# Kernel tuning notes

Measured on AMD Instinct MI355X. Metric: run time of the kernel, lower is better.

The kernel has to match this reference:

```python
import jax, jax.numpy as jnp
import numpy as np

R = 4
D = 2 * R + 1  # 9
B, C, H, W = 1, 256, 48, 96


def setup_inputs() -> dict:
    key = jax.random.key(0)
    k1, k2, k3, k4, k5 = jax.random.split(key, 5)
    f1 = jax.random.normal(k1, (B, C, H, W), dtype=jnp.float32)
    f2 = jax.random.normal(k2, (B, C, H, W), dtype=jnp.float32)
    cx = jax.random.uniform(k3, (B, H, W), dtype=jnp.float32) * (W - 1)
    cy = jax.random.uniform(k4, (B, H, W), dtype=jnp.float32) * (H - 1)
    coords = jnp.stack([cx, cy], axis=1)  # (B,2,H,W), ch0=x, ch1=y
    # DAP: 1x1 conv over (2r+1)^2 channels, identity init (perturbed so it is non-trivial)
    w_dap = jnp.eye(D * D, dtype=jnp.float32) + 0.02 * jax.random.normal(k5, (D * D, D * D), dtype=jnp.float32)
    return {"f1": f1, "f2": f2, "coords": coords, "w_dap": w_dap}


def _bilinear_sample(img, px, py):
    # img: (C,H,W); px,py: (M,) pixel coords; zeros padding, align_corners=True semantics
    c, h, w = img.shape
    x0 = jnp.floor(px)
    y0 = jnp.floor(py)
    x1 = x0 + 1.0
    y1 = y0 + 1.0
    wx1 = px - x0
    wx0 = 1.0 - wx1
    wy1 = py - y0
    wy0 = 1.0 - wy1
    flat = img.reshape(c, h * w)

    def corner(xi, yi, wgt):
        valid = (xi >= 0) & (xi <= w - 1) & (yi >= 0) & (yi <= h - 1)
        xc = jnp.clip(xi, 0, w - 1).astype(jnp.int32)
        yc = jnp.clip(yi, 0, h - 1).astype(jnp.int32)
        v = flat[:, yc * w + xc]  # (C,M)
        return v * (wgt * valid.astype(wgt.dtype))[None, :]

    return (corner(x0, y0, wx0 * wy0) + corner(x1, y0, wx1 * wy0)
            + corner(x0, y1, wx0 * wy1) + corner(x1, y1, wx1 * wy1))


def _corr_forward(f1, f2, coords, w_dap):
    b, c, h, w = f1.shape
    d = jnp.linspace(-R, R, D, dtype=f1.dtype)
    # centroids[b, i, y, j, x] = (coords_x + dx[i], coords_y + dy[j])
    px = coords[:, 0][:, None, :, None, :] + d[None, :, None, None, None]  # (B,D,H,1,W)->(B,D,H,D,W)
    py = coords[:, 1][:, None, :, None, :] + d[None, None, None, :, None]
    px = jnp.broadcast_to(px, (b, D, h, D, w)).reshape(b, -1)
    py = jnp.broadcast_to(py, (b, D, h, D, w)).reshape(b, -1)
    samp = jax.vmap(_bilinear_sample)(f2, px, py)  # (B, C, D*H*D*W)
    f2s = samp.reshape(b, c, D, h, D, w)
    corr = jnp.einsum('bcihjw,bchw->bijhw', f2s, f1) / jnp.sqrt(jnp.asarray(c, f1.dtype))
    cf = corr.reshape(b, D * D, h, w)
    out = jnp.einsum('od,bdhw->bohw', w_dap, cf)  # DAP 1x1 conv, no bias
    return out  # (B, (2r+1)^2, H, W)


def reference(f1, f2, coords, w_dap):
    return _corr_forward(f1, f2, coords, w_dap)
```

## Files before the change

kernel.cpp:

```cpp
#include <hip/hip_runtime.h>

#define HH   48
#define WW   96
#define CC   256
#define DD   9
#define DD2  81
#define HWSZ (HH * WW)
#define ROWB 512
#define ZOFF ((unsigned)HWSZ * ROWB)
#define NCX  24
#define NCY  24
#define NCELL (NCX * NCY)
#define HROWS 143
#define HRP   144
#define HROWB 256
#define CAP  32
#define CBL_STR 104

typedef __attribute__((ext_vector_type(8))) short short8v;
typedef __attribute__((ext_vector_type(4))) float f32x4;

__device__ __forceinline__ unsigned bf16rne(float f) {
  unsigned u = __float_as_uint(f);
  return (u + 0x7FFFu + ((u >> 16) & 1u)) >> 16;
}

__device__ __forceinline__ void gload_lds16(const char* g, char* l) {
  __builtin_amdgcn_global_load_lds(
      (const __attribute__((address_space(1))) char*)g,
      (__attribute__((address_space(3))) char*)l, 16, 0, 0);
}

__global__ __launch_bounds__(256) void transpose_to_bf16(
    const float* __restrict__ f1, const float* __restrict__ f2,
    const float* __restrict__ w_dap, const float* __restrict__ coords,
    char* __restrict__ f2tb, char* __restrict__ f1tb, char* __restrict__ zpage,
    unsigned short* __restrict__ Wf, int* __restrict__ cnt,
    int* __restrict__ plist) {
  __shared__ float tile[64][65];
  const float* src = (blockIdx.y == 0) ? f1 : f2;
  char* dst = (blockIdx.y == 0) ? f1tb : f2tb;

  const int tid = threadIdx.x;
  if (blockIdx.y == 0 && blockIdx.x == 0 && tid < 32) {
    float4 z = {0.f, 0.f, 0.f, 0.f};
    *(float4*)(zpage + tid * 16) = z;
  }
  if (blockIdx.y == 0 && blockIdx.x < 36) {
    int gid = blockIdx.x * 256 + tid;
    int g = gid >> 9;
    int idx = gid & 511;
    int ln = idx >> 3, e = idx & 7;
    int m = g / 3, kt = g - m * 3;
    int r = m * 16 + (ln & 15);
    int c = kt * 32 + (ln >> 4) * 8 + e;
    float v = (r < DD2 && c < DD2) ? w_dap[r * DD2 + c] : 0.f;
    Wf[gid] = (unsigned short)bf16rne(v);
  }
  if (blockIdx.y == 1 && blockIdx.x < 18) {
    const int p = blockIdx.x * 256 + tid;
    const int ix = (int)coords[p];
    const int iy = (int)coords[HWSZ + p];
    const int cell = (iy >> 1) * NCX + (ix >> 2);
    const int slot = atomicAdd(&cnt[cell], 1);
    if (slot < CAP) plist[cell * CAP + slot] = p;
  }

  const int tiles_p = HWSZ / 64;
  const int bc = blockIdx.x / tiles_p;
  const int bp = blockIdx.x % tiles_p;
  const int c0 = bc * 64, p0 = bp * 64;

#pragma unroll
  for (int k = 0; k < 16; k++) {
    int idx = k * 256 + tid;
    int cl = idx >> 6, pl = idx & 63;
    tile[cl][pl] = src[(size_t)(c0 + cl) * HWSZ + p0 + pl];
  }
  __syncthreads();
#pragma unroll
  for (int k = 0; k < 8; k++) {
    int idx = k * 256 + tid;
    int pl = idx >> 5, cp = idx & 31;
    unsigned lo = bf16rne(tile[2 * cp][pl]);
    unsigned hi = bf16rne(tile[2 * cp + 1][pl]);
    *(unsigned*)(dst + (size_t)(p0 + pl) * ROWB + (size_t)c0 * 2 + cp * 4) =
        lo | (hi << 16);
  }
}

__global__ __launch_bounds__(256, 3) void corr_region(
    const char* __restrict__ f2tb, const char* __restrict__ f1tb,
    const float* __restrict__ coords, const int* __restrict__ cnt,
    const int* __restrict__ plist, const unsigned short* __restrict__ Wf,
    float* __restrict__ out) {
  __shared__ __align__(16) char halo[HRP * HROWB];
  __shared__ float dsf[HRP * 16];
  __shared__ unsigned rowoff[HRP];
  __shared__ __align__(16) unsigned short cbl[16 * CBL_STR];

  const int cell = blockIdx.x;
  const int ci = cell % NCX, cj = cell / NCX;
  const int npix0 = cnt[cell];
  const int npix = npix0 < CAP ? npix0 : CAP;
  if (npix == 0) return;

  const int tid = threadIdx.x;
  const int lane = tid & 63, wid = tid >> 6;
  const int hi = lane >> 4, lo = lane & 15;

  const int hx0 = ci * 4 - 4, hy0 = cj * 2 - 4;

  if (tid < HRP) {
    unsigned ro = ZOFF;
    if (tid < HROWS) {
      const int hy = (tid * 158) >> 11;
      const int hx = tid - hy * 13;
      const int gy = hy0 + hy, gx = hx0 + hx;
      if (gx >= 0 && gx < WW && gy >= 0 && gy < HH)
        ro = (unsigned)(gy * WW + gx) * ROWB;
    }
    rowoff[tid] = ro;
  }
  __syncthreads();

  const int nb = (npix + 15) >> 4;
  for (int b = 0; b < nb; ++b) {
    const int slot = b * 16 + lo;
    const bool valid = slot < npix;
    const int pi = valid ? plist[cell * CAP + slot] : 0;
    const char* fb = valid ? (f1tb + (size_t)pi * ROWB) : (f2tb + ZOFF);
    short8v bq[8];
#pragma unroll
    for (int kt = 0; kt < 8; kt++)
      bq[kt] = *(const short8v*)(fb + kt * 64 + hi * 16);

    f32x4 acc0 = {0.f, 0.f, 0.f, 0.f};
    f32x4 acc1 = {0.f, 0.f, 0.f, 0.f};
    f32x4 acc2 = {0.f, 0.f, 0.f, 0.f};

#pragma unroll
    for (int pass = 0; pass < 2; pass++) {
      for (int s = wid; s < 36; s += 4) {
        const int r = 4 * s + hi;
        gload_lds16(
            f2tb + rowoff[r] + pass * 256 + ((lo * 16) ^ ((r & 7) << 4)),
            &halo[s * 1024]);
      }
      __syncthreads();

      {
        const int rr = wid * 16 + lo;
        const int swz = (rr & 7) << 4;
        const char* rp = halo + rr * HROWB;
        short8v a0 = *(const short8v*)(rp + ((hi * 16 + 0) ^ swz));
        short8v a1 = *(const short8v*)(rp + ((hi * 16 + 64) ^ swz));
        short8v a2 = *(const short8v*)(rp + ((hi * 16 + 128) ^ swz));
        short8v a3 = *(const short8v*)(rp + ((hi * 16 + 192) ^ swz));
        acc0 = __builtin_amdgcn_mfma_f32_16x16x32_bf16(a0, bq[pass * 4 + 0], acc0, 0, 0, 0);
        acc0 = __builtin_amdgcn_mfma_f32_16x16x32_bf16(a1, bq[pass * 4 + 1], acc0, 0, 0, 0);
        acc0 = __builtin_amdgcn_mfma_f32_16x16x32_bf16(a2, bq[pass * 4 + 2], acc0, 0, 0, 0);
        acc0 = __builtin_amdgcn_mfma_f32_16x16x32_bf16(a3, bq[pass * 4 + 3], acc0, 0, 0, 0);
      }
      {
        const int rr = (wid + 4) * 16 + lo;
        const int swz = (rr & 7) << 4;
        const char* rp = halo + rr * HROWB;
        short8v a0 = *(const short8v*)(rp + ((hi * 16 + 0) ^ swz));
        short8v a1 = *(const short8v*)(rp + ((hi * 16 + 64) ^ swz));
        short8v a2 = *(const short8v*)(rp + ((hi * 16 + 128) ^ swz));
        short8v a3 = *(const short8v*)(rp + ((hi * 16 + 192) ^ swz));
        acc1 = __builtin_amdgcn_mfma_f32_16x16x32_bf16(a0, bq[pass * 4 + 0], acc1, 0, 0, 0);
        acc1 = __builtin_amdgcn_mfma_f32_16x16x32_bf16(a1, bq[pass * 4 + 1], acc1, 0, 0, 0);
        acc1 = __builtin_amdgcn_mfma_f32_16x16x32_bf16(a2, bq[pass * 4 + 2], acc1, 0, 0, 0);
        acc1 = __builtin_amdgcn_mfma_f32_16x16x32_bf16(a3, bq[pass * 4 + 3], acc1, 0, 0, 0);
      }
      if (wid == 0) {
        const int rr = 8 * 16 + lo;
        const int swz = (rr & 7) << 4;
        const char* rp = halo + rr * HROWB;
        short8v a0 = *(const short8v*)(rp + ((hi * 16 + 0) ^ swz));
        short8v a1 = *(const short8v*)(rp + ((hi * 16 + 64) ^ swz));
        short8v a2 = *(const short8v*)(rp + ((hi * 16 + 128) ^ swz));
        short8v a3 = *(const short8v*)(rp + ((hi * 16 + 192) ^ swz));
        acc2 = __builtin_amdgcn_mfma_f32_16x16x32_bf16(a0, bq[pass * 4 + 0], acc2, 0, 0, 0);
        acc2 = __builtin_amdgcn_mfma_f32_16x16x32_bf16(a1, bq[pass * 4 + 1], acc2, 0, 0, 0);
        acc2 = __builtin_amdgcn_mfma_f32_16x16x32_bf16(a2, bq[pass * 4 + 2], acc2, 0, 0, 0);
        acc2 = __builtin_amdgcn_mfma_f32_16x16x32_bf16(a3, bq[pass * 4 + 3], acc2, 0, 0, 0);
      }
      __syncthreads();
    }

#pragma unroll
    for (int j = 0; j < 4; j++)
      dsf[(wid * 16 + hi * 4 + j) * 16 + lo] = acc0[j];
#pragma unroll
    for (int j = 0; j < 4; j++)
      dsf[((wid + 4) * 16 + hi * 4 + j) * 16 + lo] = acc1[j];
    if (wid == 0) {
#pragma unroll
      for (int j = 0; j < 4; j++)
        dsf[(8 * 16 + hi * 4 + j) * 16 + lo] = acc2[j];
    }
    __syncthreads();

    {
      const int s2 = tid & 15;
      const int g = tid >> 4;
      const int slot2 = b * 16 + s2;
      if (slot2 < npix) {
        const int pi2 = plist[cell * CAP + slot2];
        const float cx = coords[pi2];
        const float cy = coords[HWSZ + pi2];
        const float fxf = floorf(cx), fyf = floorf(cy);
        const float fx = cx - fxf, fy = cy - fyf;
        const int ox = (int)fxf - ci * 4;
        const int oy = (int)fyf - cj * 2;
#pragma unroll
        for (int e = 0; e < 6; e++) {
          const int o = g * 6 + e;
          float cv = 0.f;
          if (o < DD2) {
            const int i = o / DD, j = o - i * DD;
            const int rb = (oy + j) * 13 + ox + i;
            const float d00 = dsf[rb * 16 + s2];
            const float d01 = dsf[(rb + 1) * 16 + s2];
            const float d10 = dsf[(rb + 13) * 16 + s2];
            const float d11 = dsf[(rb + 14) * 16 + s2];
            cv = ((1.f - fy) * ((1.f - fx) * d00 + fx * d01) +
                  fy * ((1.f - fx) * d10 + fx * d11)) * 0.0625f;
          }
          cbl[s2 * CBL_STR + o] = (unsigned short)bf16rne(cv);
        }
      }
    }
    __syncthreads();

    {
      short8v bq2[3];
#pragma unroll
      for (int kt = 0; kt < 3; kt++)
        bq2[kt] = *(const short8v*)&cbl[lo * CBL_STR + kt * 32 + hi * 8];
      const int slot3 = b * 16 + lo;
      const bool v3 = slot3 < npix;
      const int po = v3 ? plist[cell * CAP + slot3] : 0;
#pragma unroll
      for (int mi = 0; mi < 2; mi++) {
        const int m = wid + mi * 4;
        if (m < 6) {
          f32x4 acc = {0.f, 0.f, 0.f, 0.f};
#pragma unroll
          for (int kt = 0; kt < 3; kt++) {
            short8v aw = *(const short8v*)(Wf + ((size_t)(m * 3 + kt) * 64 + lane) * 8);
            acc = __builtin_amdgcn_mfma_f32_16x16x32_bf16(aw, bq2[kt], acc, 0, 0, 0);
          }
          if (v3) {
#pragma unroll
            for (int j = 0; j < 4; j++) {
              const int o = m * 16 + hi * 4 + j;
              if (o < DD2) out[(size_t)o * HWSZ + po] = acc[j];
            }
          }
        }
      }
    }
    if (b + 1 < nb) __syncthreads();
  }
}

extern "C" void kernel_launch(void* const* d_in, const int* in_sizes, int n_in,
                              void* d_out, int out_size, void* d_ws, size_t ws_size,
                              hipStream_t stream) {
  const float* f1     = (const float*)d_in[0];
  const float* f2     = (const float*)d_in[1];
  const float* coords = (const float*)d_in[2];
  const float* w_dap  = (const float*)d_in[3];
  float* out = (float*)d_out;

  char* f2tb  = (char*)d_ws;
  char* zpage = f2tb + (size_t)HWSZ * ROWB;
  char* f1tb  = zpage + 512;
  unsigned short* Wf = (unsigned short*)(f1tb + (size_t)HWSZ * ROWB);
  int* cnt   = (int*)(Wf + 9216);
  int* plist = cnt + NCELL;

  hipMemsetAsync(cnt, 0, NCELL * sizeof(int), stream);

  dim3 tgrid((CC / 64) * (HWSZ / 64), 2);
  transpose_to_bf16<<<tgrid, 256, 0, stream>>>(f1, f2, w_dap, coords, f2tb, f1tb,
                                               zpage, Wf, cnt, plist);

  corr_region<<<dim3(NCELL), 256, 0, stream>>>(f2tb, f1tb, coords, cnt, plist, Wf, out);
}
```

Baseline: 29.64 us.

## Halve LDS halo chunk to raise occupancy and vectorize transpose kernel

The correlation kernel now stages the f2 halo in 128-byte channel chunks over four passes instead of 256-byte chunks over two. This halves the halo LDS footprint so launch bounds can target four blocks per SM, adjusting the load mapping and swizzle to match. The cost is twice as many barrier-separated load/compute phases per pixel batch. Separately, the transpose kernel switches to float4 global loads and 16-byte bf16 stores to cut memory instruction count.

```diff
diff --git a/kernel.cpp b/kernel.cpp
--- a/kernel.cpp
+++ b/kernel.cpp
@@ -13,7 +13,7 @@
 #define NCELL (NCX * NCY)
 #define HROWS 143
 #define HRP   144
-#define HROWB 256
+#define HROWB 128
 #define CAP  32
 #define CBL_STR 104
 
@@ -37,7 +37,7 @@
     char* __restrict__ f2tb, char* __restrict__ f1tb, char* __restrict__ zpage,
     unsigned short* __restrict__ Wf, int* __restrict__ cnt,
     int* __restrict__ plist) {
-  __shared__ float tile[64][65];
+  __shared__ __align__(16) float tile[64][68];
   const float* src = (blockIdx.y == 0) ? f1 : f2;
   char* dst = (blockIdx.y == 0) ? f1tb : f2tb;
 
@@ -72,24 +72,33 @@
   const int c0 = bc * 64, p0 = bp * 64;
 
 #pragma unroll
-  for (int k = 0; k < 16; k++) {
+  for (int k = 0; k < 4; k++) {
     int idx = k * 256 + tid;
-    int cl = idx >> 6, pl = idx & 63;
-    tile[cl][pl] = src[(size_t)(c0 + cl) * HWSZ + p0 + pl];
+    int cl = idx >> 4, q = idx & 15;
+    float4 v = *(const float4*)(src + (size_t)(c0 + cl) * HWSZ + p0 + q * 4);
+    *(float4*)&tile[cl][q * 4] = v;
   }
   __syncthreads();
-#pragma unroll
-  for (int k = 0; k < 8; k++) {
-    int idx = k * 256 + tid;
-    int pl = idx >> 5, cp = idx & 31;
-    unsigned lo = bf16rne(tile[2 * cp][pl]);
-    unsigned hi = bf16rne(tile[2 * cp + 1][pl]);
-    *(unsigned*)(dst + (size_t)(p0 + pl) * ROWB + (size_t)c0 * 2 + cp * 4) =
-        lo | (hi << 16);
-  }
-}
-
-__global__ __launch_bounds__(256, 3) void corr_region(
+  {
+    const int px = tid >> 2, part = tid & 3;
+    unsigned w[8];
+#pragma unroll
+    for (int j = 0; j < 8; j++) {
+      unsigned lo = bf16rne(tile[part * 16 + 2 * j][px]);
+      unsigned hi = bf16rne(tile[part * 16 + 2 * j + 1][px]);
+      w[j] = lo | (hi << 16);
+    }
+    char* dp = dst + (size_t)(p0 + px) * ROWB + c0 * 2 + part * 32;
+    float4 v0 = {__uint_as_float(w[0]), __uint_as_float(w[1]),
+                 __uint_as_float(w[2]), __uint_as_float(w[3])};
+    float4 v1 = {__uint_as_float(w[4]), __uint_as_float(w[5]),
+                 __uint_as_float(w[6]), __uint_as_float(w[7])};
+    *(float4*)dp = v0;
+    *(float4*)(dp + 16) = v1;
+  }
+}
+
+__global__ __launch_bounds__(256, 4) void corr_region(
     const char* __restrict__ f2tb, const char* __restrict__ f1tb,
     const float* __restrict__ coords, const int* __restrict__ cnt,
     const int* __restrict__ plist, const unsigned short* __restrict__ Wf,
@@ -124,6 +133,9 @@
   }
   __syncthreads();
 
+  const int srow = lane >> 3;
+  const int sOff = ((lane & 7) * 16) ^ (srow << 4);
+
   const int nb = (npix + 15) >> 4;
   for (int b = 0; b < nb; ++b) {
     const int slot = b * 16 + lo;
@@ -140,12 +152,10 @@
     f32x4 acc2 = {0.f, 0.f, 0.f, 0.f};
 
 #pragma unroll
-    for (int pass = 0; pass < 2; pass++) {
-      for (int s = wid; s < 36; s += 4) {
-        const int r = 4 * s + hi;
-        gload_lds16(
-            f2tb + rowoff[r] + pass * 256 + ((lo * 16) ^ ((r & 7) << 4)),
-            &halo[s * 1024]);
+    for (int pass = 0; pass < 4; pass++) {
+      for (int s = wid; s < 18; s += 4) {
+        const int r = 8 * s + srow;
+        gload_lds16(f2tb + rowoff[r] + pass * 128 + sOff, &halo[s * 1024]);
       }
       __syncthreads();
 
@@ -153,40 +163,28 @@
         const int rr = wid * 16 + lo;
         const int swz = (rr & 7) << 4;
         const char* rp = halo + rr * HROWB;
-        short8v a0 = *(const short8v*)(rp + ((hi * 16 + 0) ^ swz));
+        short8v a0 = *(const short8v*)(rp + ((hi * 16) ^ swz));
         short8v a1 = *(const short8v*)(rp + ((hi * 16 + 64) ^ swz));
-        short8v a2 = *(const short8v*)(rp + ((hi * 16 + 128) ^ swz));
-        short8v a3 = *(const short8v*)(rp + ((hi * 16 + 192) ^ swz));
-        acc0 = __builtin_amdgcn_mfma_f32_16x16x32_bf16(a0, bq[pass * 4 + 0], acc0, 0, 0, 0);
-        acc0 = __builtin_amdgcn_mfma_f32_16x16x32_bf16(a1, bq[pass * 4 + 1], acc0, 0, 0, 0);
-        acc0 = __builtin_amdgcn_mfma_f32_16x16x32_bf16(a2, bq[pass * 4 + 2], acc0, 0, 0, 0);
-        acc0 = __builtin_amdgcn_mfma_f32_16x16x32_bf16(a3, bq[pass * 4 + 3], acc0, 0, 0, 0);
+        acc0 = __builtin_amdgcn_mfma_f32_16x16x32_bf16(a0, bq[pass * 2 + 0], acc0, 0, 0, 0);
+        acc0 = __builtin_amdgcn_mfma_f32_16x16x32_bf16(a1, bq[pass * 2 + 1], acc0, 0, 0, 0);
       }
       {
         const int rr = (wid + 4) * 16 + lo;
         const int swz = (rr & 7) << 4;
         const char* rp = halo + rr * HROWB;
-        short8v a0 = *(const short8v*)(rp + ((hi * 16 + 0) ^ swz));
+        short8v a0 = *(const short8v*)(rp + ((hi * 16) ^ swz));
         short8v a1 = *(const short8v*)(rp + ((hi * 16 + 64) ^ swz));
-        short8v a2 = *(const short8v*)(rp + ((hi * 16 + 128) ^ swz));
-        short8v a3 = *(const short8v*)(rp + ((hi * 16 + 192) ^ swz));
-        acc1 = __builtin_amdgcn_mfma_f32_16x16x32_bf16(a0, bq[pass * 4 + 0], acc1, 0, 0, 0);
-        acc1 = __builtin_amdgcn_mfma_f32_16x16x32_bf16(a1, bq[pass * 4 + 1], acc1, 0, 0, 0);
-        acc1 = __builtin_amdgcn_mfma_f32_16x16x32_bf16(a2, bq[pass * 4 + 2], acc1, 0, 0, 0);
-        acc1 = __builtin_amdgcn_mfma_f32_16x16x32_bf16(a3, bq[pass * 4 + 3], acc1, 0, 0, 0);
+        acc1 = __builtin_amdgcn_mfma_f32_16x16x32_bf16(a0, bq[pass * 2 + 0], acc1, 0, 0, 0);
+        acc1 = __builtin_amdgcn_mfma_f32_16x16x32_bf16(a1, bq[pass * 2 + 1], acc1, 0, 0, 0);
       }
       if (wid == 0) {
         const int rr = 8 * 16 + lo;
         const int swz = (rr & 7) << 4;
         const char* rp = halo + rr * HROWB;
-        short8v a0 = *(const short8v*)(rp + ((hi * 16 + 0) ^ swz));
+        short8v a0 = *(const short8v*)(rp + ((hi * 16) ^ swz));
         short8v a1 = *(const short8v*)(rp + ((hi * 16 + 64) ^ swz));
-        short8v a2 = *(const short8v*)(rp + ((hi * 16 + 128) ^ swz));
-        short8v a3 = *(const short8v*)(rp + ((hi * 16 + 192) ^ swz));
-        acc2 = __builtin_amdgcn_mfma_f32_16x16x32_bf16(a0, bq[pass * 4 + 0], acc2, 0, 0, 0);
-        acc2 = __builtin_amdgcn_mfma_f32_16x16x32_bf16(a1, bq[pass * 4 + 1], acc2, 0, 0, 0);
-        acc2 = __builtin_amdgcn_mfma_f32_16x16x32_bf16(a2, bq[pass * 4 + 2], acc2, 0, 0, 0);
-        acc2 = __builtin_amdgcn_mfma_f32_16x16x32_bf16(a3, bq[pass * 4 + 3], acc2, 0, 0, 0);
+        acc2 = __builtin_amdgcn_mfma_f32_16x16x32_bf16(a0, bq[pass * 2 + 0], acc2, 0, 0, 0);
+        acc2 = __builtin_amdgcn_mfma_f32_16x16x32_bf16(a1, bq[pass * 2 + 1], acc2, 0, 0, 0);
       }
       __syncthreads();
     }
```

After: 30.97 us. 4.5% more time.
